# Kernel optimization log

Hardware: AMD Instinct MI355X
Metric: run time of the kernel (lower is better)

Reference implementation:

```python
import jax, jax.numpy as jnp
import numpy as np

N_NODES = 100000
N_EDGES = 1600000
D = 128          # h_size == feature_representation_size
N_CLASSES = 2
N_GRAPHS = 64


def setup_inputs() -> dict:
    key = jax.random.key(0)
    ks = jax.random.split(key, 8)
    scale = 1.0 / np.sqrt(D)
    x = jax.random.normal(ks[0], (N_NODES, D), jnp.float32)
    edge_index = jax.random.randint(ks[1], (2, N_EDGES), 0, N_NODES, dtype=jnp.int64)
    batch = jnp.sort(jax.random.randint(ks[2], (N_NODES,), 0, N_GRAPHS, dtype=jnp.int64))
    W0 = jax.random.normal(ks[3], (D, D), jnp.float32) * scale
    W1 = jax.random.normal(ks[4], (D, D), jnp.float32) * scale
    W2 = jax.random.normal(ks[5], (D, D), jnp.float32) * scale
    Wf = jax.random.normal(ks[6], (D, N_CLASSES), jnp.float32) * scale
    return dict(
        x=x, edge_index=edge_index, batch=batch,
        W0=W0, b0=jnp.zeros((D,), jnp.float32),
        W1=W1, b1=jnp.zeros((D,), jnp.float32),
        W2=W2, b2=jnp.zeros((D,), jnp.float32),
        Wf=Wf, bf=jnp.zeros((N_CLASSES,), jnp.float32),
    )


def gcn_norm(edge_index, num_nodes):
    # add self loops, symmetric normalization D^{-1/2} A_hat D^{-1/2}
    src, dst = edge_index[0], edge_index[1]
    loop = jnp.arange(num_nodes, dtype=src.dtype)
    src = jnp.concatenate([src, loop])
    dst = jnp.concatenate([dst, loop])
    ew = jnp.ones(src.shape[0], jnp.float32)
    deg = jax.ops.segment_sum(ew, dst, num_segments=num_nodes)
    dinv = jnp.where(deg > 0, jax.lax.rsqrt(deg), 0.0)
    norm = dinv[src] * dinv[dst]  # [E+N]
    return src, dst, norm


def gcn_conv(h, W, b, src, dst, norm, num_nodes):
    h = h @ W                                   # linear transform
    msg = h[src] * norm[:, None]                # gather + scale over edges
    out = jax.ops.segment_sum(msg, dst, num_segments=num_nodes)  # scatter-add
    return out + b


def reference(x, edge_index, batch, W0, b0, W1, b1, W2, b2, Wf, bf):
    n = x.shape[0]
    src, dst, norm = gcn_norm(edge_index, n)
    h = jax.nn.relu(gcn_conv(x, W0, b0, src, dst, norm, n))
    h = jax.nn.relu(gcn_conv(h, W1, b1, src, dst, norm, n))
    h = gcn_conv(h, W2, b2, src, dst, norm, n)  # last layer, no relu
    pooled = jax.ops.segment_max(h, batch, num_segments=N_GRAPHS)  # global max pool
    return pooled @ Wf + bf
```

## Files before the change

### kernel.cpp

```cpp
#include <hip/hip_runtime.h>
#include <hip/hip_bf16.h>
#include <hip/hip_fp16.h>
#include <float.h>

#define D 128
#define NGRAPHS 64
#define BKSHIFT 9
#define BKNODES 512
#define MAXBK 256
#define PCH 4096

typedef _Float16 h8 __attribute__((ext_vector_type(8)));
typedef float f4 __attribute__((ext_vector_type(4)));

__device__ __forceinline__ unsigned fkey(float f){
  unsigned u = __float_as_uint(f);
  return (u & 0x80000000u) ? ~u : (u | 0x80000000u);
}
__device__ __forceinline__ float funkey(unsigned k){
  unsigned u = (k & 0x80000000u) ? (k ^ 0x80000000u) : ~k;
  return __uint_as_float(u);
}

__global__ __launch_bounds__(256) void k_bhist(const int* __restrict__ dst,
    int* __restrict__ bcnt, int E){
  __shared__ int h[MAXBK];
  int t = threadIdx.x;
  for (int i = t; i < MAXBK; i += 256) h[i] = 0;
  __syncthreads();
  int e0 = blockIdx.x * PCH;
  #pragma unroll
  for (int j = 0; j < PCH / 256; j++){
    int e = e0 + t + j * 256;
    if (e < E) atomicAdd(&h[dst[e] >> BKSHIFT], 1);
  }
  __syncthreads();
  for (int i = t; i < MAXBK; i += 256) if (h[i]) atomicAdd(&bcnt[i], h[i]);
}

__global__ __launch_bounds__(256) void k_bscan(const int* __restrict__ bcnt,
    int* __restrict__ bOff, int* __restrict__ bCur, int* __restrict__ row_ptr,
    int nbk, int N, int E){
  __shared__ int sh[256];
  int t = threadIdx.x;
  int v = (t < nbk) ? bcnt[t] : 0;
  sh[t] = v; __syncthreads();
  for (int off = 1; off < 256; off <<= 1){
    int x = (t >= off) ? sh[t - off] : 0;
    __syncthreads();
    sh[t] += x;
    __syncthreads();
  }
  if (t < nbk){ int ex = sh[t] - v; bOff[t] = ex; bCur[t] = ex; }
  if (t == 0){ bOff[nbk] = E; row_ptr[N] = E; }
}

__global__ __launch_bounds__(256) void k_part(const int* __restrict__ src,
    const int* __restrict__ dst, int* __restrict__ bCur,
    uint2* __restrict__ epart, int E){
  __shared__ int scnt[MAXBK], soff[MAXBK], sbase[MAXBK], scur[MAXBK];
  __shared__ int stmp[256];
  __shared__ uint2 stage[PCH];
  int t = threadIdx.x;
  int e0 = blockIdx.x * PCH;
  int eN = E - e0; if (eN > PCH) eN = PCH;
  for (int i = t; i < MAXBK; i += 256){ scnt[i] = 0; scur[i] = 0; }
  __syncthreads();
  uint2 mye[PCH / 256];
  #pragma unroll
  for (int j = 0; j < PCH / 256; j++){
    int e = e0 + t + j * 256;
    if (e < E){
      mye[j].x = (unsigned)src[e];
      mye[j].y = (unsigned)dst[e];
      atomicAdd(&scnt[mye[j].y >> BKSHIFT], 1);
    }
  }
  __syncthreads();
  int v = scnt[t];
  stmp[t] = v; __syncthreads();
  for (int off = 1; off < 256; off <<= 1){
    int x = (t >= off) ? stmp[t - off] : 0;
    __syncthreads();
    stmp[t] += x;
    __syncthreads();
  }
  soff[t] = stmp[t] - v;
  if (v > 0) sbase[t] = atomicAdd(&bCur[t], v);
  __syncthreads();
  #pragma unroll
  for (int j = 0; j < PCH / 256; j++){
    int e = e0 + t + j * 256;
    if (e < E){
      int b = mye[j].y >> BKSHIFT;
      int l = atomicAdd(&scur[b], 1);
      stage[soff[b] + l] = mye[j];
    }
  }
  __syncthreads();
  for (int j = t; j < eN; j += 256){
    uint2 ed = stage[j];
    int b = (int)(ed.y >> BKSHIFT);
    epart[(size_t)sbase[b] + (j - soff[b])] = ed;
  }
}

__global__ __launch_bounds__(256) void k_bfill(const uint2* __restrict__ epart,
    const int* __restrict__ bOff, int* __restrict__ row_ptr,
    int* __restrict__ col, float* __restrict__ dinv, int N){
  __shared__ int hc[BKNODES], off[BKNODES], cur[BKNODES];
  __shared__ int stmp[256];
  int b = blockIdx.x, t = threadIdx.x;
  int base = bOff[b], cntE = bOff[b + 1] - base;
  int node0 = b << BKSHIFT;
  int nloc = N - node0; if (nloc > BKNODES) nloc = BKNODES;
  for (int i = t; i < BKNODES; i += 256) hc[i] = 0;
  __syncthreads();
  for (int j = t; j < cntE; j += 256){
    uint2 ed = epart[(size_t)base + j];
    atomicAdd(&hc[ed.y - node0], 1);
  }
  __syncthreads();
  int a0 = hc[2 * t], a1 = hc[2 * t + 1];
  int s = a0 + a1;
  stmp[t] = s; __syncthreads();
  for (int o = 1; o < 256; o <<= 1){
    int x = (t >= o) ? stmp[t - o] : 0;
    __syncthreads();
    stmp[t] += x;
    __syncthreads();
  }
  int ex = stmp[t] - s;
  off[2 * t] = ex; off[2 * t + 1] = ex + a0;
  __syncthreads();
  for (int i = t; i < nloc; i += 256){
    row_ptr[node0 + i] = base + off[i];
    dinv[node0 + i]    = rsqrtf((float)hc[i] + 1.0f);
    cur[i] = off[i];
  }
  __syncthreads();
  for (int j = t; j < cntE; j += 256){
    uint2 ed = epart[(size_t)base + j];
    int p = atomicAdd(&cur[ed.y - node0], 1);
    col[base + p] = (int)ed.x;
  }
}

__global__ __launch_bounds__(256) void k_cvt(const float* __restrict__ in,
    _Float16* __restrict__ outp, int n8){
  int i = blockIdx.x * 256 + threadIdx.x;
  if (i >= n8) return;
  float4 a = *(const float4*)&in[(size_t)i * 8];
  float4 b = *(const float4*)&in[(size_t)i * 8 + 4];
  __half2 p0 = __floats2half2_rn(a.x, a.y);
  __half2 p1 = __floats2half2_rn(a.z, a.w);
  __half2 p2 = __floats2half2_rn(b.x, b.y);
  __half2 p3 = __floats2half2_rn(b.z, b.w);
  uint4 u;
  u.x = *(unsigned*)&p0; u.y = *(unsigned*)&p1;
  u.z = *(unsigned*)&p2; u.w = *(unsigned*)&p3;
  *(uint4*)&outp[(size_t)i * 8] = u;
}

__global__ __launch_bounds__(256) void k_wcvt3(const float* __restrict__ W0,
    const float* __restrict__ W1, const float* __restrict__ W2,
    _Float16* __restrict__ Wsw){
  const float* W = (blockIdx.x == 0) ? W0 : (blockIdx.x == 1) ? W1 : W2;
  _Float16* dst = Wsw + (size_t)blockIdx.x * 16384;
  int lane = threadIdx.x & 63;
  int quad = lane >> 4;
  int n    = lane & 15;
  for (int pair = (threadIdx.x >> 6); pair < 32; pair += 4){
    int k0 = pair >> 3;
    int tt = pair & 7;
    _Float16 v[8];
    #pragma unroll
    for (int j = 0; j < 8; j++){
      int k = k0 * 32 + quad * 8 + j;
      v[j] = (_Float16)W[k * 128 + 16 * tt + n];
    }
    *(uint4*)&dst[((size_t)pair * 64 + lane) * 8] = *(uint4*)v;
  }
}

__global__ __launch_bounds__(256) void gemm_mfma(const _Float16* __restrict__ A,
    const _Float16* __restrict__ Wsw, _Float16* __restrict__ C, int M){
  __shared__ _Float16 lds[4][16][136];
  int wave = threadIdx.x >> 6;
  int lane = threadIdx.x & 63;
  int quad = lane >> 4;
  int l15  = lane & 15;
  int m0 = blockIdx.x * 64 + wave * 16;
  if (m0 >= M) return;
  f4 acc[8] = {};
  h8 af[4];
  const _Float16* arow = A + (size_t)(m0 + l15) * D;
  #pragma unroll
  for (int k0 = 0; k0 < 4; k0++)
    af[k0] = *(const h8*)&arow[k0 * 32 + quad * 8];
  #pragma unroll
  for (int k0 = 0; k0 < 4; k0++){
    #pragma unroll
    for (int t = 0; t < 8; t++){
      h8 bf = *(const h8*)&Wsw[((size_t)(k0 * 8 + t) * 64 + lane) * 8];
      acc[t] = __builtin_amdgcn_mfma_f32_16x16x32_f16(af[k0], bf, acc[t], 0, 0, 0);
    }
  }
  #pragma unroll
  for (int t = 0; t < 8; t++){
    #pragma unroll
    for (int r = 0; r < 4; r++)
      lds[wave][quad * 4 + r][t * 16 + l15] = (_Float16)acc[t][r];
  }
  #pragma unroll
  for (int it = 0; it < 4; it++){
    int idx = it * 64 + lane;
    int row = idx >> 4;
    int ch  = idx & 15;
    *(uint4*)&C[(size_t)(m0 + row) * D + ch * 8] = *(uint4*)&lds[wave][row][ch * 8];
  }
}

__device__ __forceinline__ void accm(float* acc, uint4 u, float w){
  union { uint4 u; _Float16 h[8]; } cv;
  cv.u = u;
  #pragma unroll
  for (int k = 0; k < 8; k++)
    acc[k] += (float)cv.h[k] * w;
}

__global__ __launch_bounds__(256) void k_agg(const __half* __restrict__ t,
    const int* __restrict__ row_ptr, const int* __restrict__ col,
    const float* __restrict__ dinv, const float* __restrict__ bias,
    __half* __restrict__ outh, int relu, int N){
  int node = blockIdx.x * 4 + (threadIdx.x >> 6);
  if (node >= N) return;
  int lane = threadIdx.x & 63;
  int way  = lane >> 4;
  int cg   = (lane & 15) * 8;
  float di = dinv[node];
  int beg = row_ptr[node], end = row_ptr[node + 1];
  float acc[8] = {0.f,0.f,0.f,0.f,0.f,0.f,0.f,0.f};
  int j = beg + way;
  for (; j + 12 < end; j += 16){
    int s0 = col[j], s1 = col[j + 4], s2 = col[j + 8], s3 = col[j + 12];
    float w0 = dinv[s0] * di;
    float w1 = dinv[s1] * di;
    float w2 = dinv[s2] * di;
    float w3 = dinv[s3] * di;
    uint4 u0 = *(const uint4*)&t[(size_t)s0 * D + cg];
    uint4 u1 = *(const uint4*)&t[(size_t)s1 * D + cg];
    uint4 u2 = *(const uint4*)&t[(size_t)s2 * D + cg];
    uint4 u3 = *(const uint4*)&t[(size_t)s3 * D + cg];
    accm(acc, u0, w0);
    accm(acc, u1, w1);
    accm(acc, u2, w2);
    accm(acc, u3, w3);
  }
  for (; j < end; j += 4){
    int s = col[j];
    float w = dinv[s] * di;
    uint4 u = *(const uint4*)&t[(size_t)s * D + cg];
    accm(acc, u, w);
  }
  #pragma unroll
  for (int k = 0; k < 8; k++){
    acc[k] += __shfl_xor(acc[k], 16, 64);
    acc[k] += __shfl_xor(acc[k], 32, 64);
  }
  if (way == 0){
    uint4 su = *(const uint4*)&t[(size_t)node * D + cg];
    union { uint4 u; _Float16 h[8]; } sv; sv.u = su;
    float dii = di * di;
    float4 b0 = *(const float4*)&bias[cg];
    float4 b1 = *(const float4*)&bias[cg + 4];
    float bb[8] = {b0.x, b0.y, b0.z, b0.w, b1.x, b1.y, b1.z, b1.w};
    float o[8];
    #pragma unroll
    for (int k = 0; k < 8; k++)
      o[k] = acc[k] + (float)sv.h[k] * dii + bb[k];
    if (relu){
      #pragma unroll
      for (int k = 0; k < 8; k++) o[k] = fmaxf(o[k], 0.f);
    }
    __half2 p0 = __floats2half2_rn(o[0], o[1]);
    __half2 p1 = __floats2half2_rn(o[2], o[3]);
    __half2 p2 = __floats2half2_rn(o[4], o[5]);
    __half2 p3 = __floats2half2_rn(o[6], o[7]);
    uint4 u;
    u.x = *(unsigned*)&p0; u.y = *(unsigned*)&p1;
    u.z = *(unsigned*)&p2; u.w = *(unsigned*)&p3;
    *(uint4*)&outh[(size_t)node * D + cg] = u;
  }
}

__global__ __launch_bounds__(128) void k_pool(const __half* __restrict__ h,
    const int* __restrict__ batch, unsigned* __restrict__ pk, int N){
  int d = threadIdx.x;
  int n0 = blockIdx.x * 128;
  int nEnd = n0 + 128; if (nEnd > N) nEnd = N;
  float cur = -FLT_MAX;
  int curg = batch[n0];
  for (int n = n0; n < nEnd; n++){
    int g = batch[n];
    if (g != curg){
      atomicMax(&pk[curg * D + d], fkey(cur));
      cur = -FLT_MAX; curg = g;
    }
    cur = fmaxf(cur, __half2float(h[(size_t)n * D + d]));
  }
  atomicMax(&pk[curg * D + d], fkey(cur));
}

__global__ __launch_bounds__(128) void k_final(const unsigned* __restrict__ pk,
    const float* __restrict__ Wf, const float* __restrict__ bf,
    float* __restrict__ out){
  int t = threadIdx.x;
  int g = t >> 1, c = t & 1;
  float s = bf[c];
  for (int k = 0; k < D; k++)
    s += funkey(pk[g * D + k]) * Wf[k * 2 + c];
  out[g * 2 + c] = s;
}

extern "C" void kernel_launch(void* const* d_in, const int* in_sizes, int n_in,
                              void* d_out, int out_size, void* d_ws, size_t ws_size,
                              hipStream_t stream){
  const float* x   = (const float*)d_in[0];
  const int*   ei  = (const int*)d_in[1];
  const int*   bat = (const int*)d_in[2];
  const float* W0  = (const float*)d_in[3];
  const float* b0  = (const float*)d_in[4];
  const float* W1  = (const float*)d_in[5];
  const float* b1  = (const float*)d_in[6];
  const float* W2  = (const float*)d_in[7];
  const float* b2  = (const float*)d_in[8];
  const float* Wf  = (const float*)d_in[9];
  const float* bf  = (const float*)d_in[10];
  int N = in_sizes[0] / D;
  int E = in_sizes[1] / 2;
  const int* srcp = ei;
  const int* dstp = ei + E;
  int nbk   = (N + BKNODES - 1) / BKNODES;
  int npart = (E + PCH - 1) / PCH;

  char* p = (char*)d_ws;
  auto alloc = [&](size_t bytes)->char*{
    char* r = p; p += (bytes + 255) & ~(size_t)255; return r;
  };
  float*     dinv    = (float*)alloc((size_t)N * 4);
  int*       row_ptr = (int*)alloc((size_t)(N + 1) * 4);
  int*       col     = (int*)alloc((size_t)E * 4);
  uint2*     epart   = (uint2*)alloc((size_t)E * 8);
  _Float16*  tmp     = (_Float16*)alloc((size_t)N * D * 2);
  _Float16*  h16     = (_Float16*)alloc((size_t)N * D * 2);
  _Float16*  Wsw     = (_Float16*)alloc((size_t)3 * 16384 * 2);
  unsigned*  pk      = (unsigned*)alloc((size_t)NGRAPHS * D * 4);
  int*       bcnt    = (int*)alloc((size_t)MAXBK * 4);
  int*       bOff    = (int*)alloc((size_t)(MAXBK + 1) * 4);
  int*       bCur    = (int*)alloc((size_t)MAXBK * 4);

  hipMemsetAsync(bcnt, 0, (size_t)MAXBK * 4, stream);
  hipMemsetAsync(pk, 0, (size_t)NGRAPHS * D * 4, stream);

  int n8 = N * D / 8;
  k_cvt<<<(n8 + 255) / 256, 256, 0, stream>>>(x, h16, n8);
  k_wcvt3<<<3, 256, 0, stream>>>(W0, W1, W2, Wsw);

  k_bhist<<<npart, 256, 0, stream>>>(dstp, bcnt, E);
  k_bscan<<<1, 256, 0, stream>>>(bcnt, bOff, bCur, row_ptr, nbk, N, E);
  k_part<<<npart, 256, 0, stream>>>(srcp, dstp, bCur, epart, E);
  k_bfill<<<nbk, 256, 0, stream>>>(epart, bOff, row_ptr, col, dinv, N);

  int gblocks = (N + 63) / 64;
  int ablocks = (N + 3) / 4;
  gemm_mfma<<<gblocks, 256, 0, stream>>>(h16, Wsw, tmp, N);
  k_agg<<<ablocks, 256, 0, stream>>>((const __half*)tmp, row_ptr, col, dinv, b0, (__half*)h16, 1, N);
  gemm_mfma<<<gblocks, 256, 0, stream>>>(h16, Wsw + 16384, tmp, N);
  k_agg<<<ablocks, 256, 0, stream>>>((const __half*)tmp, row_ptr, col, dinv, b1, (__half*)h16, 1, N);
  gemm_mfma<<<gblocks, 256, 0, stream>>>(h16, Wsw + 32768, tmp, N);
  k_agg<<<ablocks, 256, 0, stream>>>((const __half*)tmp, row_ptr, col, dinv, b2, (__half*)h16, 0, N);
  k_pool<<<(N + 127) / 128, 128, 0, stream>>>((const __half*)h16, bat, pk, N);
  k_final<<<1, 128, 0, stream>>>(pk, Wf, bf, (float*)d_out);
}
```

Measured before the change: 450.3 us.

## Fuse input conversion into first GEMM and merge small setup kernels

Drops the separate fp32-to-fp16 pass over x: the first layer's GEMM now reads fp32 rows and converts them in registers. Weight conversion moves into spare blocks of the histogram kernel, and clearing the pooling buffer moves into the scan kernel, which removes two launches and a memset. The pooling kernel takes half as many nodes per block and unrolls its loop four ways so more loads are in flight. The first GEMM now reads twice as many bytes of x in exchange for skipping a full write and re-read of the fp16 copy.

```diff
diff --git a/kernel.cpp b/kernel.cpp
--- a/kernel.cpp
+++ b/kernel.cpp
@@ -22,8 +22,30 @@
   return __uint_as_float(u);
 }
 
-__global__ __launch_bounds__(256) void k_bhist(const int* __restrict__ dst,
-    int* __restrict__ bcnt, int E){
+__global__ __launch_bounds__(256) void k_bhist_w(const int* __restrict__ dst,
+    int* __restrict__ bcnt, int E, int npart,
+    const float* __restrict__ W0, const float* __restrict__ W1,
+    const float* __restrict__ W2, _Float16* __restrict__ Wsw){
+  if ((int)blockIdx.x >= npart){
+    int layer = blockIdx.x - npart;
+    const float* W = (layer == 0) ? W0 : (layer == 1) ? W1 : W2;
+    _Float16* dstp = Wsw + (size_t)layer * 16384;
+    int lane = threadIdx.x & 63;
+    int quad = lane >> 4;
+    int n    = lane & 15;
+    for (int pair = (threadIdx.x >> 6); pair < 32; pair += 4){
+      int k0 = pair >> 3;
+      int tt = pair & 7;
+      _Float16 v[8];
+      #pragma unroll
+      for (int j = 0; j < 8; j++){
+        int k = k0 * 32 + quad * 8 + j;
+        v[j] = (_Float16)W[k * 128 + 16 * tt + n];
+      }
+      *(uint4*)&dstp[((size_t)pair * 64 + lane) * 8] = *(uint4*)v;
+    }
+    return;
+  }
   __shared__ int h[MAXBK];
   int t = threadIdx.x;
   for (int i = t; i < MAXBK; i += 256) h[i] = 0;
@@ -40,9 +62,10 @@
 
 __global__ __launch_bounds__(256) void k_bscan(const int* __restrict__ bcnt,
     int* __restrict__ bOff, int* __restrict__ bCur, int* __restrict__ row_ptr,
-    int nbk, int N, int E){
+    unsigned* __restrict__ pk, int nbk, int N, int E){
   __shared__ int sh[256];
   int t = threadIdx.x;
+  for (int i = t; i < NGRAPHS * D; i += 256) pk[i] = 0u;
   int v = (t < nbk) ? bcnt[t] : 0;
   sh[t] = v; __syncthreads();
   for (int off = 1; off < 256; off <<= 1){
@@ -143,43 +166,6 @@
     uint2 ed = epart[(size_t)base + j];
     int p = atomicAdd(&cur[ed.y - node0], 1);
     col[base + p] = (int)ed.x;
-  }
-}
-
-__global__ __launch_bounds__(256) void k_cvt(const float* __restrict__ in,
-    _Float16* __restrict__ outp, int n8){
-  int i = blockIdx.x * 256 + threadIdx.x;
-  if (i >= n8) return;
-  float4 a = *(const float4*)&in[(size_t)i * 8];
-  float4 b = *(const float4*)&in[(size_t)i * 8 + 4];
-  __half2 p0 = __floats2half2_rn(a.x, a.y);
-  __half2 p1 = __floats2half2_rn(a.z, a.w);
-  __half2 p2 = __floats2half2_rn(b.x, b.y);
-  __half2 p3 = __floats2half2_rn(b.z, b.w);
-  uint4 u;
-  u.x = *(unsigned*)&p0; u.y = *(unsigned*)&p1;
-  u.z = *(unsigned*)&p2; u.w = *(unsigned*)&p3;
-  *(uint4*)&outp[(size_t)i * 8] = u;
-}
-
-__global__ __launch_bounds__(256) void k_wcvt3(const float* __restrict__ W0,
-    const float* __restrict__ W1, const float* __restrict__ W2,
-    _Float16* __restrict__ Wsw){
-  const float* W = (blockIdx.x == 0) ? W0 : (blockIdx.x == 1) ? W1 : W2;
-  _Float16* dst = Wsw + (size_t)blockIdx.x * 16384;
-  int lane = threadIdx.x & 63;
-  int quad = lane >> 4;
-  int n    = lane & 15;
-  for (int pair = (threadIdx.x >> 6); pair < 32; pair += 4){
-    int k0 = pair >> 3;
-    int tt = pair & 7;
-    _Float16 v[8];
-    #pragma unroll
-    for (int j = 0; j < 8; j++){
-      int k = k0 * 32 + quad * 8 + j;
-      v[j] = (_Float16)W[k * 128 + 16 * tt + n];
-    }
-    *(uint4*)&dst[((size_t)pair * 64 + lane) * 8] = *(uint4*)v;
   }
 }
 
@@ -198,6 +184,54 @@
   #pragma unroll
   for (int k0 = 0; k0 < 4; k0++)
     af[k0] = *(const h8*)&arow[k0 * 32 + quad * 8];
+  #pragma unroll
+  for (int k0 = 0; k0 < 4; k0++){
+    #pragma unroll
+    for (int t = 0; t < 8; t++){
+      h8 bf = *(const h8*)&Wsw[((size_t)(k0 * 8 + t) * 64 + lane) * 8];
+      acc[t] = __builtin_amdgcn_mfma_f32_16x16x32_f16(af[k0], bf, acc[t], 0, 0, 0);
+    }
+  }
+  #pragma unroll
+  for (int t = 0; t < 8; t++){
+    #pragma unroll
+    for (int r = 0; r < 4; r++)
+      lds[wave][quad * 4 + r][t * 16 + l15] = (_Float16)acc[t][r];
+  }
+  #pragma unroll
+  for (int it = 0; it < 4; it++){
+    int idx = it * 64 + lane;
+    int row = idx >> 4;
+    int ch  = idx & 15;
+    *(uint4*)&C[(size_t)(m0 + row) * D + ch * 8] = *(uint4*)&lds[wave][row][ch * 8];
+  }
+}
+
+__global__ __launch_bounds__(256) void gemm_mfma_f32A(const float* __restrict__ A,
+    const _Float16* __restrict__ Wsw, _Float16* __restrict__ C, int M){
+  __shared__ _Float16 lds[4][16][136];
+  int wave = threadIdx.x >> 6;
+  int lane = threadIdx.x & 63;
+  int quad = lane >> 4;
+  int l15  = lane & 15;
+  int m0 = blockIdx.x * 64 + wave * 16;
+  if (m0 >= M) return;
+  f4 acc[8] = {};
+  h8 af[4];
+  const float* arow = A + (size_t)(m0 + l15) * D;
+  #pragma unroll
+  for (int k0 = 0; k0 < 4; k0++){
+    float4 a = *(const float4*)&arow[k0 * 32 + quad * 8];
+    float4 b = *(const float4*)&arow[k0 * 32 + quad * 8 + 4];
+    __half2 p0 = __floats2half2_rn(a.x, a.y);
+    __half2 p1 = __floats2half2_rn(a.z, a.w);
+    __half2 p2 = __floats2half2_rn(b.x, b.y);
+    __half2 p3 = __floats2half2_rn(b.z, b.w);
+    union { uint4 u; h8 v; } cv;
+    cv.u.x = *(unsigned*)&p0; cv.u.y = *(unsigned*)&p1;
+    cv.u.z = *(unsigned*)&p2; cv.u.w = *(unsigned*)&p3;
+    af[k0] = cv.v;
+  }
   #pragma unroll
   for (int k0 = 0; k0 < 4; k0++){
     #pragma unroll
@@ -297,16 +331,27 @@
 __global__ __launch_bounds__(128) void k_pool(const __half* __restrict__ h,
     const int* __restrict__ batch, unsigned* __restrict__ pk, int N){
   int d = threadIdx.x;
-  int n0 = blockIdx.x * 128;
-  int nEnd = n0 + 128; if (nEnd > N) nEnd = N;
+  int n0 = blockIdx.x * 64;
+  int nEnd = n0 + 64; if (nEnd > N) nEnd = N;
   float cur = -FLT_MAX;
   int curg = batch[n0];
-  for (int n = n0; n < nEnd; n++){
+  int n = n0;
+  for (; n + 3 < nEnd; n += 4){
+    const __half* r = &h[(size_t)n * D + d];
+    __half v0 = r[0], v1 = r[D], v2 = r[2 * D], v3 = r[3 * D];
+    int g0 = batch[n], g1 = batch[n + 1], g2 = batch[n + 2], g3 = batch[n + 3];
+    if (g0 != curg){ atomicMax(&pk[curg * D + d], fkey(cur)); cur = -FLT_MAX; curg = g0; }
+    cur = fmaxf(cur, __half2float(v0));
+    if (g1 != curg){ atomicMax(&pk[curg * D + d], fkey(cur)); cur = -FLT_MAX; curg = g1; }
+    cur = fmaxf(cur, __half2float(v1));
+    if (g2 != curg){ atomicMax(&pk[curg * D + d], fkey(cur)); cur = -FLT_MAX; curg = g2; }
+    cur = fmaxf(cur, __half2float(v2));
+    if (g3 != curg){ atomicMax(&pk[curg * D + d], fkey(cur)); cur = -FLT_MAX; curg = g3; }
+    cur = fmaxf(cur, __half2float(v3));
+  }
+  for (; n < nEnd; n++){
     int g = batch[n];
-    if (g != curg){
-      atomicMax(&pk[curg * D + d], fkey(cur));
-      cur = -FLT_MAX; curg = g;
-    }
+    if (g != curg){ atomicMax(&pk[curg * D + d], fkey(cur)); cur = -FLT_MAX; curg = g; }
     cur = fmaxf(cur, __half2float(h[(size_t)n * D + d]));
   }
   atomicMax(&pk[curg * D + d], fkey(cur));
@@ -361,25 +406,20 @@
   int*       bCur    = (int*)alloc((size_t)MAXBK * 4);
 
   hipMemsetAsync(bcnt, 0, (size_t)MAXBK * 4, stream);
-  hipMemsetAsync(pk, 0, (size_t)NGRAPHS * D * 4, stream);
-
-  int n8 = N * D / 8;
-  k_cvt<<<(n8 + 255) / 256, 256, 0, stream>>>(x, h16, n8);
-  k_wcvt3<<<3, 256, 0, stream>>>(W0, W1, W2, Wsw);
-
-  k_bhist<<<npart, 256, 0, stream>>>(dstp, bcnt, E);
-  k_bscan<<<1, 256, 0, stream>>>(bcnt, bOff, bCur, row_ptr, nbk, N, E);
+
+  k_bhist_w<<<npart + 3, 256, 0, stream>>>(dstp, bcnt, E, npart, W0, W1, W2, Wsw);
+  k_bscan<<<1, 256, 0, stream>>>(bcnt, bOff, bCur, row_ptr, pk, nbk, N, E);
   k_part<<<npart, 256, 0, stream>>>(srcp, dstp, bCur, epart, E);
   k_bfill<<<nbk, 256, 0, stream>>>(epart, bOff, row_ptr, col, dinv, N);
 
   int gblocks = (N + 63) / 64;
   int ablocks = (N + 3) / 4;
-  gemm_mfma<<<gblocks, 256, 0, stream>>>(h16, Wsw, tmp, N);
+  gemm_mfma_f32A<<<gblocks, 256, 0, stream>>>(x, Wsw, tmp, N);
   k_agg<<<ablocks, 256, 0, stream>>>((const __half*)tmp, row_ptr, col, dinv, b0, (__half*)h16, 1, N);
   gemm_mfma<<<gblocks, 256, 0, stream>>>(h16, Wsw + 16384, tmp, N);
   k_agg<<<ablocks, 256, 0, stream>>>((const __half*)tmp, row_ptr, col, dinv, b1, (__half*)h16, 1, N);
   gemm_mfma<<<gblocks, 256, 0, stream>>>(h16, Wsw + 32768, tmp, N);
   k_agg<<<ablocks, 256, 0, stream>>>((const __half*)tmp, row_ptr, col, dinv, b2, (__half*)h16, 0, N);
-  k_pool<<<(N + 127) / 128, 128, 0, stream>>>((const __half*)h16, bat, pk, N);
+  k_pool<<<(N + 63) / 64, 128, 0, stream>>>((const __half*)h16, bat, pk, N);
   k_final<<<1, 128, 0, stream>>>(pk, Wf, bf, (float*)d_out);
 }
```

After: 412.5 us. 1.09x faster.
